# Performance work log

Measured on AMD Instinct MI355X. Metric: run time of the kernel, lower is better.

## Reference

```python
import math
import jax, jax.numpy as jnp
import numpy as np

EPS = 1e-6
MAX_SCALE_LOG = math.log(100.0)

def rms_norm(x, scale, eps=EPS):
    # x * scale / rms(x), reduction over last dim
    ms = jnp.mean(jnp.square(x), axis=-1, keepdims=True)
    return x * (scale * jax.lax.rsqrt(ms + eps))

def axial_rope_theta(pos, n_heads, d_head, dtype):
    # freqs: linspace in log-space from pi to 10*pi, reshaped to [n_heads, d_head//4]
    f = np.exp(np.linspace(math.log(math.pi), math.log(10.0 * math.pi),
                           n_heads * d_head // 4 + 1)[:-1])
    freqs = jnp.asarray(f.reshape(d_head // 4, n_heads).T, dtype)  # [h, e/4]
    theta_h = pos[:, :, None, 0:1] * freqs  # [n, l, h, e/4]
    theta_w = pos[:, :, None, 1:2] * freqs  # [n, l, h, e/4]
    theta = jnp.concatenate([theta_h, theta_w], axis=-1)  # [n, l, h, e/2]
    return theta.transpose(0, 2, 1, 3)  # [n, h, l, e/2]

def apply_rotary(x, theta):
    d = theta.shape[-1]
    x1, x2, x3 = x[..., :d], x[..., d:2 * d], x[..., 2 * d:]
    cos, sin = jnp.cos(theta), jnp.sin(theta)
    return jnp.concatenate([x1 * cos - x2 * sin, x2 * cos + x1 * sin, x3], axis=-1)

def setup_inputs() -> dict:
    key = jax.random.key(0)
    ks = jax.random.split(key, 8)
    n, l, d_model, d_head = 2, 2048, 1024, 64
    n_heads = d_model // d_head
    x = jax.random.normal(ks[0], (n, l, d_model), jnp.float32)
    pos = jax.random.uniform(ks[1], (n, l, 2), jnp.float32)
    cond = jax.random.normal(ks[2], (n, 1, d_model), jnp.float32)
    # params (torch uses zero-init for w_cond/w_out; small random for a non-degenerate baseline)
    w_cond = jax.random.normal(ks[3], (d_model, d_model), jnp.float32) * 0.02
    w_qkv = jax.random.normal(ks[4], (d_model, 3 * d_model), jnp.float32) * (d_model ** -0.5)
    qk_scale = jnp.full((n_heads,), math.log(10.0), jnp.float32)
    w_out = jax.random.normal(ks[5], (d_model, d_model), jnp.float32) * 0.02
    return {"x": x, "pos": pos, "cond": cond, "w_cond": w_cond,
            "w_qkv": w_qkv, "qk_scale": qk_scale, "w_out": w_out}

def reference(x, pos, cond, w_cond, w_qkv, qk_scale, w_out):
    n, l, d_model = x.shape
    h = qk_scale.shape[0]
    e = d_model // h
    # AdaRMSNorm: scale = linear(cond) + 1
    xn = rms_norm(x, cond @ w_cond + 1.0)
    # QKV projection
    q, k, v = jnp.split(xn @ w_qkv, 3, axis=-1)
    to_heads = lambda t: t.reshape(n, l, h, e).transpose(0, 2, 1, 3)  # [n,h,l,e]
    q, k, v = to_heads(q), to_heads(k), to_heads(v)
    # QKNorm: per-head learned scale, rms over head dim
    s = jnp.exp(0.5 * jnp.minimum(qk_scale, MAX_SCALE_LOG) - 0.25 * math.log(e))
    q = rms_norm(q, s[:, None, None])
    k = rms_norm(k, s[:, None, None])
    # Axial RoPE
    theta = axial_rope_theta(pos, h, e, x.dtype)
    q = apply_rotary(q, theta)
    k = apply_rotary(k, theta)
    # SDPA (no mask)
    attn = jax.nn.softmax(jnp.einsum('nhqe,nhke->nhqk', q, k) / math.sqrt(e), axis=-1)
    o = jnp.einsum('nhqk,nhke->nhqe', attn, v)
    o = o.transpose(0, 2, 1, 3).reshape(n, l, d_model)
    return o @ w_out
```

## Files before the change

kernel.cpp:

```cpp
#include <hip/hip_runtime.h>

typedef unsigned short u16;
typedef unsigned int u32;
typedef short s16x8 __attribute__((ext_vector_type(8)));
typedef short s16x4 __attribute__((ext_vector_type(4)));
typedef float f32x4 __attribute__((ext_vector_type(4)));
typedef float f32x16 __attribute__((ext_vector_type(16)));

#define AS1 __attribute__((address_space(1)))
#define AS3 __attribute__((address_space(3)))

__device__ __forceinline__ float bf2f(u16 u) {
    union { unsigned int i; float f; } x; x.i = ((unsigned int)u) << 16; return x.f;
}
__device__ __forceinline__ u16 f2bf(float f) {
    union { float f; unsigned int i; } x; x.f = f;
    unsigned int r = (x.i + 0x7FFFu + ((x.i >> 16) & 1u)) >> 16;
    return (u16)r;
}
__device__ __forceinline__ void storeOut(u16* p, float v) { *p = f2bf(v); }
__device__ __forceinline__ void storeOut(float* p, float v) { *p = v; }
__device__ __forceinline__ float loadIn(const void* p, size_t i, int isf32) {
    return isf32 ? ((const float*)p)[i] : bf2f(((const u16*)p)[i]);
}
__device__ __forceinline__ float fexp2(float x) {
#if __has_builtin(__builtin_amdgcn_exp2f)
    return __builtin_amdgcn_exp2f(x);
#else
    return exp2f(x);
#endif
}
__device__ __forceinline__ void plswap(u32& a, u32& b) {
#if __has_builtin(__builtin_amdgcn_permlane32_swap)
    const auto r = __builtin_amdgcn_permlane32_swap(a, b, false, false);
    a = (u32)r[0]; b = (u32)r[1];
#else
    asm("v_permlane32_swap_b32 %0, %1" : "+v"(a), "+v"(b));
#endif
}

__global__ __launch_bounds__(256) void detect_dtype(const u16* __restrict__ x,
                                                    int* __restrict__ flag) {
    __shared__ int cnt[4];
    const int tid = threadIdx.x;
    int c = 0;
    #pragma unroll
    for (int i = 0; i < 4; ++i) {
        const u16 u = x[tid * 4 + i];
        const int e = (u >> 7) & 0xFF;
        c += (e >= 101 && e <= 135) ? 1 : 0;
    }
    #pragma unroll
    for (int m = 1; m < 64; m <<= 1) c += __shfl_xor(c, m, 64);
    if ((tid & 63) == 0) cnt[tid >> 6] = c;
    __syncthreads();
    if (tid == 0) {
        const int t = cnt[0] + cnt[1] + cnt[2] + cnt[3];
        *flag = (t < 800) ? 1 : 0;
    }
}

__global__ __launch_bounds__(256) void cond_gemv(const void* __restrict__ cond,
                                                 const void* __restrict__ w,
                                                 float* __restrict__ out,
                                                 const int* __restrict__ flag) {
    const int isf32 = *flag;
    const int d  = blockIdx.x * 256 + threadIdx.x;
    const int n  = blockIdx.y;
    const int k0 = blockIdx.z * 64;
    float acc = 0.f;
    #pragma unroll 8
    for (int k = 0; k < 64; ++k)
        acc += loadIn(cond, n * 1024 + k0 + k, isf32) *
               loadIn(w, (size_t)(k0 + k) * 1024 + d, isf32);
    atomicAdd(out + n * 1024 + d, acc);
}

__global__ __launch_bounds__(256) void rmsnorm_x(const void* __restrict__ x,
                                                 const float* __restrict__ scl,
                                                 u16* __restrict__ xn,
                                                 const int* __restrict__ flag) {
    const int isf32 = *flag;
    const int tok = blockIdx.x;
    const int n = tok >> 11;
    u16* orow = xn + (size_t)tok * 1024;
    const int base = threadIdx.x * 4;
    float f0, f1, f2, f3;
    if (isf32) {
        const float4 v = *(const float4*)((const float*)x + (size_t)tok * 1024 + base);
        f0 = v.x; f1 = v.y; f2 = v.z; f3 = v.w;
    } else {
        s16x4 uv = *(const s16x4*)((const u16*)x + (size_t)tok * 1024 + base);
        f0 = bf2f((u16)uv[0]); f1 = bf2f((u16)uv[1]); f2 = bf2f((u16)uv[2]); f3 = bf2f((u16)uv[3]);
    }
    float ss = f0 * f0 + f1 * f1 + f2 * f2 + f3 * f3;
    #pragma unroll
    for (int m = 1; m < 64; m <<= 1) ss += __shfl_xor(ss, m, 64);
    __shared__ float red[4];
    const int wave = threadIdx.x >> 6, lane = threadIdx.x & 63;
    if (lane == 0) red[wave] = ss;
    __syncthreads();
    float ms = (red[0] + red[1] + red[2] + red[3]) * (1.f / 1024.f);
    float rinv = rsqrtf(ms + 1e-6f);
    orow[base + 0] = f2bf(f0 * (scl[n * 1024 + base + 0] + 1.f) * rinv);
    orow[base + 1] = f2bf(f1 * (scl[n * 1024 + base + 1] + 1.f) * rinv);
    orow[base + 2] = f2bf(f2 * (scl[n * 1024 + base + 2] + 1.f) * rinv);
    orow[base + 3] = f2bf(f3 * (scl[n * 1024 + base + 3] + 1.f) * rinv);
}

__global__ __launch_bounds__(256) void transpose_bf(const void* __restrict__ src,
                                                    u16* __restrict__ dst, int R, int C,
                                                    const int* __restrict__ flag) {
    const int isf32 = *flag;
    __shared__ u16 t[32][33];
    const int c0 = blockIdx.x * 32, r0 = blockIdx.y * 32;
    const int tx = threadIdx.x & 31, ty = threadIdx.x >> 5;
    #pragma unroll
    for (int i = 0; i < 4; ++i)
        t[ty + i * 8][tx] = f2bf(loadIn(src, (size_t)(r0 + ty + i * 8) * C + c0 + tx, isf32));
    __syncthreads();
    #pragma unroll
    for (int i = 0; i < 4; ++i)
        dst[(size_t)(c0 + ty + i * 8) * R + r0 + tx] = t[tx][ty + i * 8];
}

template <typename OutT>
__global__ __launch_bounds__(256) void gemm_bt(const u16* __restrict__ A,
                                               const u16* __restrict__ BT,
                                               OutT* __restrict__ C, int Nn, int K) {
    __shared__ u16 As[128 * 32];
    __shared__ u16 Bs[128 * 32];
    const int tid = threadIdx.x;
    const int wave = tid >> 6, lane = tid & 63;
    const int l15 = lane & 15, quad = lane >> 4;
    const int bm0 = blockIdx.y * 128, bn0 = blockIdx.x * 128;
    const int wr = wave >> 1, wc = wave & 1;
    f32x4 acc[4][4] = {};
    const int srow = lane >> 2;
    const int g = (lane & 3) ^ (srow & 3);
    for (int bk = 0; bk < K; bk += 32) {
        __syncthreads();
        #pragma unroll
        for (int p = 0; p < 2; ++p) {
            const int rowl = p * 64 + wave * 16 + srow;
            const u16* ga = A + (size_t)(bm0 + rowl) * K + bk + g * 8;
            u16* la = As + (p * 64 + wave * 16) * 32;
            __builtin_amdgcn_global_load_lds((const AS1 void*)ga, (AS3 void*)la, 16, 0, 0);
            const u16* gb = BT + (size_t)(bn0 + rowl) * K + bk + g * 8;
            u16* lb = Bs + (p * 64 + wave * 16) * 32;
            __builtin_amdgcn_global_load_lds((const AS1 void*)gb, (AS3 void*)lb, 16, 0, 0);
        }
        __syncthreads();
        s16x8 af[4], bfr[4];
        #pragma unroll
        for (int mt = 0; mt < 4; ++mt) {
            const int r = wr * 64 + mt * 16 + l15;
            af[mt] = *(const s16x8*)(As + r * 32 + ((quad ^ (r & 3)) << 3));
        }
        #pragma unroll
        for (int nt = 0; nt < 4; ++nt) {
            const int r = wc * 64 + nt * 16 + l15;
            bfr[nt] = *(const s16x8*)(Bs + r * 32 + ((quad ^ (r & 3)) << 3));
        }
        #pragma unroll
        for (int mt = 0; mt < 4; ++mt)
            #pragma unroll
            for (int nt = 0; nt < 4; ++nt)
                acc[mt][nt] = __builtin_amdgcn_mfma_f32_16x16x32_bf16(af[mt], bfr[nt], acc[mt][nt], 0, 0, 0);
    }
    #pragma unroll
    for (int mt = 0; mt < 4; ++mt)
        #pragma unroll
        for (int nt = 0; nt < 4; ++nt)
            #pragma unroll
            for (int r = 0; r < 4; ++r) {
                const int row = bm0 + wr * 64 + mt * 16 + quad * 4 + r;
                const int col = bn0 + wc * 64 + nt * 16 + l15;
                storeOut(C + (size_t)row * Nn + col, acc[mt][nt][r]);
            }
}

__global__ __launch_bounds__(256) void qkv_head(const u16* __restrict__ qkv,
                                                const void* __restrict__ pos,
                                                const void* __restrict__ qk_scale,
                                                u16* __restrict__ q_ws,
                                                u16* __restrict__ k_ws,
                                                u16* __restrict__ vtg,
                                                const int* __restrict__ flag) {
    const int isf32 = *flag;
    const int nh = blockIdx.y;
    const int n = nh >> 4, h = nh & 15;
    const int l0 = blockIdx.x * 64;
    const int tid = threadIdx.x;
    const int wave = tid >> 6, lane = tid & 63;

    const float qs = loadIn(qk_scale, h, isf32);
    const float s = __expf(0.5f * fminf(qs, 4.605170186f) - 1.039720771f);
    const float qmul = s * s * 0.125f * 1.44269504089f;
    const int j = lane & 31;
    const float t = (float)((j & 15) * 16 + h);
    const float freq = 3.14159265358979f * __expf(t * (2.302585093f / 256.f));
    const int pj = j >> 4;

    #pragma unroll 2
    for (int it = 0; it < 16; ++it) {
        const int l = l0 + wave * 16 + it;
        const int tok = n * 2048 + l;
        const u16* row = qkv + (size_t)tok * 3072;
        float qv = bf2f(row[h * 64 + lane]);
        float kv = bf2f(row[1024 + h * 64 + lane]);
        float q2 = qv * qv, k2 = kv * kv;
        #pragma unroll
        for (int m = 1; m < 64; m <<= 1) { q2 += __shfl_xor(q2, m, 64); k2 += __shfl_xor(k2, m, 64); }
        float qn = qv * rsqrtf(q2 * (1.f / 64.f) + 1e-6f) * qmul;
        float kn = kv * rsqrtf(k2 * (1.f / 64.f) + 1e-6f);
        const float p = loadIn(pos, tok * 2 + pj, isf32);
        const float th = p * freq;
        const float c = __cosf(th), sn = __sinf(th);
        const float pq = __shfl_xor(qn, 32, 64);
        const float pk = __shfl_xor(kn, 32, 64);
        float qr, kr;
        if (lane < 32) { qr = qn * c - pq * sn; kr = kn * c - pk * sn; }
        else           { qr = qn * c + pq * sn; kr = kn * c + pk * sn; }
        const size_t oidx = ((size_t)nh * 2048 + l) * 64 + lane;
        q_ws[oidx] = f2bf(qr);
        k_ws[oidx] = f2bf(kr);
    }

    __shared__ u16 tbuf[64][65];
    const u16* vsrc = qkv + (size_t)(n * 2048 + l0) * 3072 + 2048 + h * 64;
    #pragma unroll
    for (int it = 0; it < 16; ++it) {
        const int idx = it * 256 + tid;
        const int r = idx >> 6, c = idx & 63;
        tbuf[r][c] = vsrc[(size_t)r * 3072 + c];
    }
    __syncthreads();
    u16* dst = vtg + (size_t)nh * 131072 + l0;
    #pragma unroll
    for (int it = 0; it < 16; ++it) {
        const int idx = it * 256 + tid;
        const int er = idx >> 6, lc = idx & 63;
        dst[(size_t)er * 2048 + lc] = tbuf[lc][er];
    }
}

__global__ __launch_bounds__(512, 2) void attn9(const u16* __restrict__ Q,
                                                const u16* __restrict__ K,
                                                const u16* __restrict__ Vtg,
                                                u16* __restrict__ O) {
    __shared__ u16 Ks[2][256 * 64];
    __shared__ u16 Vt[2][64 * 256];
    const int nh = blockIdx.y;
    const int q0 = blockIdx.x * 256;
    const int tid = threadIdx.x;
    const int wave = tid >> 6, lane = tid & 63;
    const int l31 = lane & 31, h = lane >> 5;
    const size_t hb = (size_t)nh * 2048 * 64;
    const u16* Vbase = Vtg + (size_t)nh * 131072;

    s16x8 qf[4];
    #pragma unroll
    for (int kd = 0; kd < 4; ++kd)
        qf[kd] = *(const s16x8*)(Q + hb + (size_t)(q0 + wave * 32 + l31) * 64 + kd * 16 + h * 8);

    f32x16 Oacc[2] = {};
    float lacc = 0.f;

    auto stage = [&](int ch, int slot) {
        const int kb = ch * 256;
        #pragma unroll
        for (int r = 0; r < 4; ++r) {
            const int row = r * 64 + wave * 8 + (lane >> 3);
            const int g = (lane & 7) ^ (row & 7);
            __builtin_amdgcn_global_load_lds(
                (const AS1 void*)(K + hb + (size_t)(kb + row) * 64 + g * 8),
                (AS3 void*)(Ks[slot] + (r * 64 + wave * 8) * 64), 16, 0, 0);
        }
        #pragma unroll
        for (int r = 0; r < 4; ++r) {
            const int er = (r * 8 + wave) * 2 + (lane >> 5);
            const int g2 = (lane & 31) ^ (er & 7);
            __builtin_amdgcn_global_load_lds(
                (const AS1 void*)(Vbase + (size_t)er * 2048 + kb + g2 * 8),
                (AS3 void*)(Vt[slot] + (r * 8 + wave) * 2 * 256), 16, 0, 0);
        }
    };

    stage(0, 0);

    for (int j = 0; j < 8; ++j) {
        if (j > 0) __builtin_amdgcn_s_barrier();
        if (j < 7) {
            stage(j + 1, (j + 1) & 1);
            asm volatile("s_waitcnt vmcnt(8)" ::: "memory");
        } else {
            asm volatile("s_waitcnt vmcnt(0)" ::: "memory");
        }
        __builtin_amdgcn_sched_barrier(0);
        __builtin_amdgcn_s_barrier();

        const u16* Kt = Ks[j & 1];
        const u16* Vc = Vt[j & 1];

        #pragma unroll 2
        for (int kt = 0; kt < 8; ++kt) {
            f32x16 S;
            #pragma unroll
            for (int jj = 0; jj < 16; ++jj) S[jj] = -15.f;
            const int kr = kt * 32 + l31;
            #pragma unroll
            for (int kd = 0; kd < 4; ++kd) {
                const s16x8 kf = *(const s16x8*)(Kt + kr * 64 + ((((kd << 1) + h) ^ (kr & 7)) << 3));
                S = __builtin_amdgcn_mfma_f32_32x32x16_bf16(kf, qf[kd], S, 0, 0, 0);
            }
            float e[16];
            #pragma unroll
            for (int jj = 0; jj < 16; ++jj) e[jj] = fexp2(S[jj]);
            float rs = 0.f;
            #pragma unroll
            for (int jj = 0; jj < 16; ++jj) rs += e[jj];
            lacc += rs;
            u32 c[8];
            #pragma unroll
            for (int jj = 0; jj < 8; ++jj)
                asm("v_cvt_pk_bf16_f32 %0, %1, %2" : "=v"(c[jj]) : "v"(e[2 * jj]), "v"(e[2 * jj + 1]));
            plswap(c[0], c[2]);
            plswap(c[1], c[3]);
            plswap(c[4], c[6]);
            plswap(c[5], c[7]);
            union { u32 u[4]; s16x8 v; } pfa, pfb;
            pfa.u[0] = c[0]; pfa.u[1] = c[1]; pfa.u[2] = c[2]; pfa.u[3] = c[3];
            pfb.u[0] = c[4]; pfb.u[1] = c[5]; pfb.u[2] = c[6]; pfb.u[3] = c[7];
            #pragma unroll
            for (int et = 0; et < 2; ++et) {
                const int er = et * 32 + l31;
                #pragma unroll
                for (int kdp = 0; kdp < 2; ++kdp) {
                    const int ch = kt * 4 + kdp * 2 + h;
                    const s16x8 vf = *(const s16x8*)(Vc + er * 256 + ((ch ^ (er & 7)) << 3));
                    Oacc[et] = __builtin_amdgcn_mfma_f32_32x32x16_bf16(kdp ? pfb.v : pfa.v, vf, Oacc[et], 0, 0, 0);
                }
            }
        }
    }

    lacc += __shfl_xor(lacc, 32, 64);
    const float linv_l = 1.f / lacc;
    const int n = nh >> 4, hh = nh & 15;
    #pragma unroll
    for (int r = 0; r < 16; ++r) {
        const int ql = (r & 3) + 8 * (r >> 2) + 4 * h;
        const float linv = __shfl(linv_l, ql, 64);
        const int qrow = q0 + wave * 32 + ql;
        #pragma unroll
        for (int et = 0; et < 2; ++et)
            O[((size_t)n * 2048 + qrow) * 1024 + hh * 64 + et * 32 + l31] = f2bf(Oacc[et][r] * linv);
    }
}

extern "C" void kernel_launch(void* const* d_in, const int* in_sizes, int n_in,
                              void* d_out, int out_size, void* d_ws, size_t ws_size,
                              hipStream_t stream) {
    const void* x        = d_in[0];
    const void* pos      = d_in[1];
    const void* cond     = d_in[2];
    const void* w_cond   = d_in[3];
    const void* w_qkv    = d_in[4];
    const void* qk_scale = d_in[5];
    const void* w_out    = d_in[6];

    char* ws = (char*)d_ws;
    constexpr size_t OFS_SCALE = 0;
    constexpr size_t OFS_FLAG  = 8192;
    constexpr size_t OFS_XN    = 16384;
    constexpr size_t OFS_WQKVT = OFS_XN    + 8388608;
    constexpr size_t OFS_WOUTT = OFS_WQKVT + 6291456;
    constexpr size_t OFS_QKV   = OFS_WOUTT + 2097152;
    constexpr size_t OFS_Q     = OFS_QKV   + 25165824;
    constexpr size_t OFS_K     = OFS_Q     + 8388608;
    constexpr size_t OFS_VT    = OFS_K     + 8388608;
    constexpr size_t OFS_O     = OFS_VT    + 8388608;

    float* scale = (float*)(ws + OFS_SCALE);
    int*   flag  = (int*)(ws + OFS_FLAG);
    u16* xn    = (u16*)(ws + OFS_XN);
    u16* wqkvT = (u16*)(ws + OFS_WQKVT);
    u16* woutT = (u16*)(ws + OFS_WOUTT);
    u16* qkv   = (u16*)(ws + OFS_QKV);
    u16* qws   = (u16*)(ws + OFS_Q);
    u16* kws   = (u16*)(ws + OFS_K);
    u16* vtg   = (u16*)(ws + OFS_VT);
    u16* ows   = (u16*)(ws + OFS_O);

    detect_dtype<<<dim3(1), 256, 0, stream>>>((const u16*)x, flag);
    hipMemsetAsync(scale, 0, 2 * 1024 * sizeof(float), stream);
    cond_gemv<<<dim3(4, 2, 16), 256, 0, stream>>>(cond, w_cond, scale, flag);
    rmsnorm_x<<<dim3(4096), 256, 0, stream>>>(x, scale, xn, flag);
    transpose_bf<<<dim3(96, 32), 256, 0, stream>>>(w_qkv, wqkvT, 1024, 3072, flag);
    transpose_bf<<<dim3(32, 32), 256, 0, stream>>>(w_out, woutT, 1024, 1024, flag);
    gemm_bt<u16><<<dim3(24, 32), 256, 0, stream>>>(xn, wqkvT, qkv, 3072, 1024);
    qkv_head<<<dim3(32, 32), 256, 0, stream>>>(qkv, pos, qk_scale, qws, kws, vtg, flag);
    attn9<<<dim3(8, 32), 512, 0, stream>>>(qws, kws, vtg, ows);
    gemm_bt<float><<<dim3(8, 32), 256, 0, stream>>>(ows, woutT, (float*)d_out, 1024, 1024);
}
```

Measured before the change: 230.3 us.

## Split attention key chunks across two wave groups with LDS reduction

```diff
diff --git a/kernel.cpp b/kernel.cpp
--- a/kernel.cpp
+++ b/kernel.cpp
@@ -245,16 +245,17 @@
     }
 }
 
-__global__ __launch_bounds__(512, 2) void attn9(const u16* __restrict__ Q,
-                                                const u16* __restrict__ K,
-                                                const u16* __restrict__ Vtg,
-                                                u16* __restrict__ O) {
+__global__ __launch_bounds__(1024) void attn10(const u16* __restrict__ Q,
+                                               const u16* __restrict__ K,
+                                               const u16* __restrict__ Vtg,
+                                               u16* __restrict__ O) {
     __shared__ u16 Ks[2][256 * 64];
     __shared__ u16 Vt[2][64 * 256];
     const int nh = blockIdx.y;
     const int q0 = blockIdx.x * 256;
     const int tid = threadIdx.x;
     const int wave = tid >> 6, lane = tid & 63;
+    const int wq = wave & 7, ks = wave >> 3;
     const int l31 = lane & 31, h = lane >> 5;
     const size_t hb = (size_t)nh * 2048 * 64;
     const u16* Vbase = Vtg + (size_t)nh * 131072;
@@ -262,7 +263,7 @@
     s16x8 qf[4];
     #pragma unroll
     for (int kd = 0; kd < 4; ++kd)
-        qf[kd] = *(const s16x8*)(Q + hb + (size_t)(q0 + wave * 32 + l31) * 64 + kd * 16 + h * 8);
+        qf[kd] = *(const s16x8*)(Q + hb + (size_t)(q0 + wq * 32 + l31) * 64 + kd * 16 + h * 8);
 
     f32x16 Oacc[2] = {};
     float lacc = 0.f;
@@ -270,20 +271,20 @@
     auto stage = [&](int ch, int slot) {
         const int kb = ch * 256;
         #pragma unroll
-        for (int r = 0; r < 4; ++r) {
-            const int row = r * 64 + wave * 8 + (lane >> 3);
-            const int g = (lane & 7) ^ (row & 7);
+        for (int r = 0; r < 2; ++r) {
+            const int row = r * 128 + (tid >> 3);
+            const int g = (tid & 7) ^ (row & 7);
             __builtin_amdgcn_global_load_lds(
                 (const AS1 void*)(K + hb + (size_t)(kb + row) * 64 + g * 8),
-                (AS3 void*)(Ks[slot] + (r * 64 + wave * 8) * 64), 16, 0, 0);
-        }
-        #pragma unroll
-        for (int r = 0; r < 4; ++r) {
-            const int er = (r * 8 + wave) * 2 + (lane >> 5);
+                (AS3 void*)(Ks[slot] + (r * 128 + wave * 8) * 64), 16, 0, 0);
+        }
+        #pragma unroll
+        for (int r = 0; r < 2; ++r) {
+            const int er = r * 32 + (tid >> 5);
             const int g2 = (lane & 31) ^ (er & 7);
             __builtin_amdgcn_global_load_lds(
                 (const AS1 void*)(Vbase + (size_t)er * 2048 + kb + g2 * 8),
-                (AS3 void*)(Vt[slot] + (r * 8 + wave) * 2 * 256), 16, 0, 0);
+                (AS3 void*)(Vt[slot] + (r * 32 + wave * 2) * 256), 16, 0, 0);
         }
     };
 
@@ -293,7 +294,7 @@
         if (j > 0) __builtin_amdgcn_s_barrier();
         if (j < 7) {
             stage(j + 1, (j + 1) & 1);
-            asm volatile("s_waitcnt vmcnt(8)" ::: "memory");
+            asm volatile("s_waitcnt vmcnt(4)" ::: "memory");
         } else {
             asm volatile("s_waitcnt vmcnt(0)" ::: "memory");
         }
@@ -304,16 +305,19 @@
         const u16* Vc = Vt[j & 1];
 
         #pragma unroll 2
-        for (int kt = 0; kt < 8; ++kt) {
+        for (int t = 0; t < 4; ++t) {
+            const int kt = ks * 4 + t;
             f32x16 S;
             #pragma unroll
             for (int jj = 0; jj < 16; ++jj) S[jj] = -15.f;
             const int kr = kt * 32 + l31;
+            __builtin_amdgcn_s_setprio(1);
             #pragma unroll
             for (int kd = 0; kd < 4; ++kd) {
                 const s16x8 kf = *(const s16x8*)(Kt + kr * 64 + ((((kd << 1) + h) ^ (kr & 7)) << 3));
                 S = __builtin_amdgcn_mfma_f32_32x32x16_bf16(kf, qf[kd], S, 0, 0, 0);
             }
+            __builtin_amdgcn_s_setprio(0);
             float e[16];
             #pragma unroll
             for (int jj = 0; jj < 16; ++jj) e[jj] = fexp2(S[jj]);
@@ -332,6 +336,7 @@
             union { u32 u[4]; s16x8 v; } pfa, pfb;
             pfa.u[0] = c[0]; pfa.u[1] = c[1]; pfa.u[2] = c[2]; pfa.u[3] = c[3];
             pfb.u[0] = c[4]; pfb.u[1] = c[5]; pfb.u[2] = c[6]; pfb.u[3] = c[7];
+            __builtin_amdgcn_s_setprio(1);
             #pragma unroll
             for (int et = 0; et < 2; ++et) {
                 const int er = et * 32 + l31;
@@ -342,20 +347,42 @@
                     Oacc[et] = __builtin_amdgcn_mfma_f32_32x32x16_bf16(kdp ? pfb.v : pfa.v, vf, Oacc[et], 0, 0, 0);
                 }
             }
-        }
-    }
-
-    lacc += __shfl_xor(lacc, 32, 64);
-    const float linv_l = 1.f / lacc;
-    const int n = nh >> 4, hh = nh & 15;
-    #pragma unroll
-    for (int r = 0; r < 16; ++r) {
-        const int ql = (r & 3) + 8 * (r >> 2) + 4 * h;
-        const float linv = __shfl(linv_l, ql, 64);
-        const int qrow = q0 + wave * 32 + ql;
+            __builtin_amdgcn_s_setprio(0);
+        }
+    }
+
+    __syncthreads();
+    float (*Osh)[512] = (float(*)[512]) & Ks[0][0];
+    float* Lsh = (float*)&Vt[0][0];
+    if (ks == 1) {
         #pragma unroll
         for (int et = 0; et < 2; ++et)
-            O[((size_t)n * 2048 + qrow) * 1024 + hh * 64 + et * 32 + l31] = f2bf(Oacc[et][r] * linv);
+            #pragma unroll
+            for (int r = 0; r < 16; ++r)
+                Osh[et * 16 + r][wq * 64 + lane] = Oacc[et][r];
+        Lsh[wq * 64 + lane] = lacc;
+    }
+    __syncthreads();
+    if (ks == 0) {
+        #pragma unroll
+        for (int et = 0; et < 2; ++et)
+            #pragma unroll
+            for (int r = 0; r < 16; ++r)
+                Oacc[et][r] += Osh[et * 16 + r][wq * 64 + lane];
+        lacc += Lsh[wq * 64 + lane];
+
+        lacc += __shfl_xor(lacc, 32, 64);
+        const float linv_l = 1.f / lacc;
+        const int n = nh >> 4, hh = nh & 15;
+        #pragma unroll
+        for (int r = 0; r < 16; ++r) {
+            const int ql = (r & 3) + 8 * (r >> 2) + 4 * h;
+            const float linv = __shfl(linv_l, ql, 64);
+            const int qrow = q0 + wq * 32 + ql;
+            #pragma unroll
+            for (int et = 0; et < 2; ++et)
+                O[((size_t)n * 2048 + qrow) * 1024 + hh * 64 + et * 32 + l31] = f2bf(Oacc[et][r] * linv);
+        }
     }
 }
 
@@ -401,6 +428,6 @@
     transpose_bf<<<dim3(32, 32), 256, 0, stream>>>(w_out, woutT, 1024, 1024, flag);
     gemm_bt<u16><<<dim3(24, 32), 256, 0, stream>>>(xn, wqkvT, qkv, 3072, 1024);
     qkv_head<<<dim3(32, 32), 256, 0, stream>>>(qkv, pos, qk_scale, qws, kws, vtg, flag);
-    attn9<<<dim3(8, 32), 512, 0, stream>>>(qws, kws, vtg, ows);
+    attn10<<<dim3(8, 32), 1024, 0, stream>>>(qws, kws, vtg, ows);
     gemm_bt<float><<<dim3(8, 32), 256, 0, stream>>>(ows, woutT, (float*)d_out, 1024, 1024);
 }
```

Measured after the change: 234.2 us. No clear change (+1.7%).
